# Performance work log

Measured on AMD Instinct MI355X. Metric: run time of the kernel, lower is better.

## Reference

```python
import jax, jax.numpy as jnp
import numpy as np

B, N, C = 8, 4096, 256
HEADS, SR = 8, 4
LN_EPS = 1e-5

def setup_inputs() -> dict:
    key = jax.random.key(0)
    ks = jax.random.split(key, 8)
    std = 0.02
    x = jax.random.normal(ks[0], (B, N, C), dtype=jnp.float32)
    q_w = jax.random.normal(ks[1], (C, C), dtype=jnp.float32) * std          # [in,out]
    kv_w = jax.random.normal(ks[2], (C, 2 * C), dtype=jnp.float32) * std     # [in,2*out]
    fan_out = SR * SR * C
    sr_w = jax.random.normal(ks[3], (C, C, SR, SR), dtype=jnp.float32) * np.sqrt(2.0 / fan_out)  # OIHW
    sr_b = jnp.zeros((C,), dtype=jnp.float32)
    ln_w = jnp.ones((C,), dtype=jnp.float32)
    ln_b = jnp.zeros((C,), dtype=jnp.float32)
    proj_w = jax.random.normal(ks[4], (C, C), dtype=jnp.float32) * std
    proj_b = jnp.zeros((C,), dtype=jnp.float32)
    return {"x": x, "H": 64, "W": 64, "q_w": q_w, "kv_w": kv_w, "sr_w": sr_w,
            "sr_b": sr_b, "ln_w": ln_w, "ln_b": ln_b, "proj_w": proj_w, "proj_b": proj_b}


def reference(x, H, W, q_w, kv_w, sr_w, sr_b, ln_w, ln_b, proj_w, proj_b):
    Bb, Nn, Cc = x.shape
    hd = Cc // HEADS
    scale = hd ** -0.5
    # q: [B, heads, N, hd]
    q = (x @ q_w).reshape(Bb, Nn, HEADS, hd).transpose(0, 2, 1, 3)
    # spatial reduction: conv(stride=sr) + LayerNorm
    x_ = x.transpose(0, 2, 1).reshape(Bb, Cc, H, W)
    x_ = jax.lax.conv_general_dilated(
        x_, sr_w, window_strides=(SR, SR), padding="VALID",
        dimension_numbers=("NCHW", "OIHW", "NCHW")) + sr_b[None, :, None, None]
    x_ = x_.reshape(Bb, Cc, -1).transpose(0, 2, 1)  # [B, Nk, C]
    mu = x_.mean(-1, keepdims=True)
    var = x_.var(-1, keepdims=True)
    x_ = (x_ - mu) * jax.lax.rsqrt(var + LN_EPS) * ln_w + ln_b
    # kv: [B, Nk, 2, heads, hd]
    Nk = x_.shape[1]
    kv = (x_ @ kv_w).reshape(Bb, Nk, 2, HEADS, hd)
    k = kv[:, :, 0].transpose(0, 2, 1, 3)  # [B, heads, Nk, hd]
    v = kv[:, :, 1].transpose(0, 2, 1, 3)  # [B, heads, Nk, hd]
    attn = jnp.einsum("bhnd,bhmd->bhnm", q, k) * scale
    attn = jax.nn.softmax(attn, axis=-1)
    out = jnp.einsum("bhnm,bhmd->bhnd", attn, v)  # [B, heads, N, hd]
    out = out.transpose(0, 2, 1, 3).reshape(Bb, Nn, Cc)
    return out @ proj_w + proj_b
```

## Files before the change

kernel.cpp:

```cpp
#include <hip/hip_runtime.h>
#include <hip/hip_bf16.h>
#include <math.h>

#define DI __device__ __forceinline__

static constexpr float SCALE = 0.17677669529663687f;

typedef short bf16x8 __attribute__((ext_vector_type(8)));
typedef float f32x4 __attribute__((ext_vector_type(4)));

__device__ unsigned short g_qw2[(size_t)256 * 8 * 64];
__device__ unsigned short g_kvw2[(size_t)512 * 8 * 64];
__device__ unsigned short g_pw2[(size_t)256 * 8 * 64];
__device__ unsigned short g_wt2[(size_t)256 * 128 * 64];
__device__ unsigned short g_x2[(size_t)32768 * 8 * 64];
__device__ unsigned short g_ln2[(size_t)2048 * 8 * 64];
__device__ unsigned short g_q[(size_t)64 * 4096 * 32];
__device__ unsigned short g_k[(size_t)64 * 256 * 32];
__device__ unsigned short g_vt[(size_t)64 * 32 * 256];
__device__ unsigned short g_convp[(size_t)16 * 2048 * 256];
__device__ unsigned short g_attnb[(size_t)32768 * 256];

DI float bfbits2f(unsigned short b) { return __uint_as_float(((unsigned)b) << 16); }

DI unsigned short f2bf(float f) {
  unsigned u = __float_as_uint(f);
  unsigned r = (u + 0x7fffu + ((u >> 16) & 1u)) >> 16;
  return (unsigned short)r;
}

DI float4 ld_bf4(const unsigned short* p) {
  ushort4 u = *(const ushort4*)p;
  return make_float4(bfbits2f(u.x), bfbits2f(u.y), bfbits2f(u.z), bfbits2f(u.w));
}

DI float ld1(const void* p, size_t i, int f32) {
  return f32 ? ((const float*)p)[i] : bfbits2f(((const unsigned short*)p)[i]);
}

DI float4 ld4(const void* p, size_t i, int f32) {
  if (f32) return *(const float4*)((const float*)p + i);
  return ld_bf4((const unsigned short*)p + i);
}

typedef const __attribute__((address_space(1))) void* gas_p;
typedef __attribute__((address_space(3))) void* las_p;
DI void gload16(const unsigned short* g, short* l) {
  __builtin_amdgcn_global_load_lds((gas_p)g, (las_p)l, 16, 0, 0);
}

DI int detect_f32(const void* xp) {
  const unsigned* p = (const unsigned*)xp;
  unsigned m0 = 0, m1 = 0;
#pragma unroll
  for (int i = 0; i < 32; ++i) {
    unsigned w = p[i];
    unsigned lo = w & 0x7fffu, hi = (w >> 16) & 0x7fffu;
    m0 = lo > m0 ? lo : m0;
    m1 = hi > m1 ? hi : m1;
  }
  unsigned mm = m0 > m1 ? m0 : m1;
  return mm >= 0x4680u ? 1 : 0;
}

__global__ void k_prep(const void* __restrict__ qw, const void* __restrict__ kvw,
                       const void* __restrict__ pwp, const void* __restrict__ srw,
                       const void* __restrict__ xp) {
  const int f32 = detect_f32(xp);
  int tidg = blockIdx.x * 256 + threadIdx.x;
  float v[8];
  unsigned short* dst;
  if (tidg < 8192) {
    int o = tidg >> 5, w = tidg & 31, k = w * 8;
#pragma unroll
    for (int j = 0; j < 8; ++j) v[j] = ld1(qw, (size_t)(k + j) * 256 + o, f32) * SCALE;
    dst = g_qw2 + ((size_t)o * 8 + (w >> 2)) * 64 + (w & 3) * 8;
  } else if (tidg < 24576) {
    int t = tidg - 8192;
    int o = t >> 5, w = t & 31, k = w * 8;
#pragma unroll
    for (int j = 0; j < 8; ++j) v[j] = ld1(kvw, (size_t)(k + j) * 512 + o, f32);
    dst = g_kvw2 + ((size_t)o * 8 + (w >> 2)) * 64 + (w & 3) * 8;
  } else if (tidg < 32768) {
    int t = tidg - 24576;
    int o = t >> 5, w = t & 31, k = w * 8;
#pragma unroll
    for (int j = 0; j < 8; ++j) v[j] = ld1(pwp, (size_t)(k + j) * 256 + o, f32);
    dst = g_pw2 + ((size_t)o * 8 + (w >> 2)) * 64 + (w & 3) * 8;
  } else if (tidg < 163840) {
    int t = tidg - 32768;
    int o = t >> 9, w = t & 511, k = w * 8;
#pragma unroll
    for (int j = 0; j < 8; ++j) {
      int kk = k + j, tap = kk >> 8, ci = kk & 255;
      v[j] = ld1(srw, (size_t)o * 4096 + (size_t)ci * 16 + tap, f32);
    }
    dst = g_wt2 + ((size_t)o * 128 + (w >> 2)) * 64 + (w & 3) * 8;
  } else {
    int t = tidg - 163840;
    int m = t >> 5, w = t & 31, k = w * 8;
    size_t base = (size_t)m * 256 + k;
    float4 a = ld4(xp, base, f32);
    float4 b = ld4(xp, base + 4, f32);
    v[0] = a.x; v[1] = a.y; v[2] = a.z; v[3] = a.w;
    v[4] = b.x; v[5] = b.y; v[6] = b.z; v[7] = b.w;
    dst = g_x2 + ((size_t)m * 8 + (w >> 2)) * 64 + (w & 3) * 8;
  }
  ushort4 h0, h1, l0, l1;
  h0.x = f2bf(v[0]); l0.x = f2bf(v[0] - bfbits2f(h0.x));
  h0.y = f2bf(v[1]); l0.y = f2bf(v[1] - bfbits2f(h0.y));
  h0.z = f2bf(v[2]); l0.z = f2bf(v[2] - bfbits2f(h0.z));
  h0.w = f2bf(v[3]); l0.w = f2bf(v[3] - bfbits2f(h0.w));
  h1.x = f2bf(v[4]); l1.x = f2bf(v[4] - bfbits2f(h1.x));
  h1.y = f2bf(v[5]); l1.y = f2bf(v[5] - bfbits2f(h1.y));
  h1.z = f2bf(v[6]); l1.z = f2bf(v[6] - bfbits2f(h1.z));
  h1.w = f2bf(v[7]); l1.w = f2bf(v[7] - bfbits2f(h1.w));
  *(ushort4*)dst        = h0;
  *(ushort4*)(dst + 4)  = h1;
  *(ushort4*)(dst + 32) = l0;
  *(ushort4*)(dst + 36) = l1;
}

template <int MODE>
__launch_bounds__(256, 3)
__global__ void k_mgemm(const void* __restrict__ Ax,
                        const void* __restrict__ biasp, void* __restrict__ outp) {
  constexpr bool AH = (MODE != 3);
  constexpr int ASZ = AH ? 4096 : 2048;
  __shared__ __align__(16) short smem[ASZ + 16384];
  short* sa = smem;
  short* sb = smem + ASZ;

  int f32 = 0;
  if constexpr (MODE == 3) f32 = detect_f32(Ax);

  const int tid = threadIdx.x;
  const int m0 = blockIdx.x * 64;
  const int nblk = (MODE == 2) ? blockIdx.y : 0;
  const int z = (MODE == 1) ? blockIdx.z : 0;
  const int wave = tid >> 6, lane = tid & 63;
  const int quad = lane >> 4, l15 = lane & 15;

  const int srow = tid >> 3;
  const int slot = (tid & 7) ^ (srow & 7);

  size_t abase0 = 0, abase1 = 0;
  if constexpr (MODE == 0 || MODE == 2) {
    abase0 = ((size_t)(m0 + srow) * 8) * 64 + slot * 8;
    abase1 = ((size_t)(m0 + 32 + srow) * 8) * 64 + slot * 8;
  } else if constexpr (MODE == 1) {
    const int kh = z >> 2, kw = z & 3;
#pragma unroll
    for (int r = 0; r < 2; ++r) {
      int m = m0 + r * 32 + srow;
      int bb = m >> 8, sp = m & 255;
      int oh = sp >> 4, ow = sp & 15;
      int n = (4 * oh + kh) * 64 + 4 * ow + kw;
      size_t ab = ((size_t)(bb * 4096 + n) * 8) * 64 + slot * 8;
      if (r == 0) abase0 = ab; else abase1 = ab;
    }
  } else {
    int ar = tid >> 2;
    int s3 = (tid & 3) ^ (ar & 3);
    abase0 = (size_t)(m0 + ar) * 256 + s3 * 8;
  }

  const unsigned short* Asrc =
      (MODE == 0 || MODE == 1) ? g_x2 : (MODE == 2) ? g_ln2 : g_attnb;
  const unsigned short* Bsrc = (MODE == 0) ? g_qw2 : (MODE == 1) ? g_wt2
                             : (MODE == 2) ? g_kvw2 : g_pw2;
  constexpr int NKT = (MODE == 1) ? 128 : 8;
  const size_t bbase =
      ((size_t)(nblk * 256 + srow) * NKT + (MODE == 1 ? z * 8 : 0)) * 64 + slot * 8;

  short* adst0 = sa + wave * 512 + lane * 8;
  short* adst1 = sa + 2048 + wave * 512 + lane * 8;
  short* bdst  = sb + wave * 512 + lane * 8;

  int aoff[4], boff[4];
#pragma unroll
  for (int mt = 0; mt < 4; ++mt) {
    int ar = mt * 16 + l15;
    if constexpr (AH) aoff[mt] = ar * 64 + ((quad ^ (ar & 7)) << 3);
    else              aoff[mt] = ar * 32 + ((quad ^ (ar & 3)) << 3);
  }
#pragma unroll
  for (int j = 0; j < 4; ++j) {
    int br = (4 * wave + j) * 16 + l15;
    boff[j] = br * 64 + ((quad ^ (br & 7)) << 3);
  }

  f32x4 acc[4][4] = {};

  for (int it = 0; it < 8; ++it) {
    if constexpr (AH) {
      gload16(Asrc + abase0 + it * 64, adst0);
      gload16(Asrc + abase1 + it * 64, adst1);
    } else {
      gload16(Asrc + abase0 + it * 32, adst0);
    }
#pragma unroll
    for (int r = 0; r < 8; ++r) {
      gload16(Bsrc + bbase + (size_t)r * (32 * NKT * 64) + it * 64, bdst + r * 2048);
    }
    __syncthreads();
#pragma unroll
    for (int mt = 0; mt < 4; ++mt) {
      bf16x8 a_h = *(const bf16x8*)&sa[aoff[mt]];
      bf16x8 a_l;
      if constexpr (AH) a_l = *(const bf16x8*)&sa[aoff[mt] ^ 32];
#pragma unroll
      for (int j = 0; j < 4; ++j) {
        bf16x8 b_h = *(const bf16x8*)&sb[boff[j]];
        bf16x8 b_l = *(const bf16x8*)&sb[boff[j] ^ 32];
        f32x4 c = acc[mt][j];
        c = __builtin_amdgcn_mfma_f32_16x16x32_bf16(a_h, b_h, c, 0, 0, 0);
        if constexpr (AH)
          c = __builtin_amdgcn_mfma_f32_16x16x32_bf16(a_l, b_h, c, 0, 0, 0);
        c = __builtin_amdgcn_mfma_f32_16x16x32_bf16(a_h, b_l, c, 0, 0, 0);
        acc[mt][j] = c;
      }
    }
    __syncthreads();
  }

  const int f32o = f32;
#pragma unroll
  for (int mt = 0; mt < 4; ++mt) {
#pragma unroll
    for (int j = 0; j < 4; ++j) {
#pragma unroll
      for (int r = 0; r < 4; ++r) {
        int m = m0 + mt * 16 + quad * 4 + r;
        int c = nblk * 256 + (4 * wave + j) * 16 + l15;
        float v = acc[mt][j][r];
        if constexpr (MODE == 0) {
          int b = m >> 12, n = m & 4095;
          int h = c >> 5, d = c & 31;
          g_q[(((size_t)(b * 8 + h) * 4096 + n) << 5) + d] = f2bf(v);
        } else if constexpr (MODE == 1) {
          g_convp[((size_t)blockIdx.z * 2048 + m) * 256 + c] = f2bf(v);
        } else if constexpr (MODE == 2) {
          int s = c >> 8, h = (c >> 5) & 7, d = c & 31;
          int bb = m >> 8, nk = m & 255;
          if (s == 0)
            g_k[(((size_t)(bb * 8 + h) * 256 + nk) << 5) + d] = f2bf(v);
          else
            g_vt[(((size_t)(bb * 8 + h) * 32 + d) << 8) + nk] = f2bf(v);
        } else {
          float rr = v + ld1(biasp, c, f32o);
          if (f32o) ((float*)outp)[(size_t)m * 256 + c] = rr;
          else      ((unsigned short*)outp)[(size_t)m * 256 + c] = f2bf(rr);
        }
      }
    }
  }
}

__global__ void k_redln(const void* __restrict__ xp, const void* __restrict__ srb,
                        const void* __restrict__ lw, const void* __restrict__ lb) {
  const int f32 = detect_f32(xp);
  int row = blockIdx.x, t = threadIdx.x;
  size_t idx = (size_t)row * 256 + t;
  float v = 0.f;
#pragma unroll
  for (int z = 0; z < 16; ++z) v += bfbits2f(g_convp[(size_t)z * (2048 * 256) + idx]);
  v += ld1(srb, t, f32);
  float s = v, sq = v * v;
#pragma unroll
  for (int off = 32; off >= 1; off >>= 1) {
    s += __shfl_down(s, off, 64);
    sq += __shfl_down(sq, off, 64);
  }
  __shared__ float rs[4], rq[4];
  int wid = t >> 6;
  if ((t & 63) == 0) { rs[wid] = s; rq[wid] = sq; }
  __syncthreads();
  float st = rs[0] + rs[1] + rs[2] + rs[3];
  float qt = rq[0] + rq[1] + rq[2] + rq[3];
  float mu = st * (1.0f / 256.0f);
  float var = qt * (1.0f / 256.0f) - mu * mu;
  float r = rsqrtf(var + 1e-5f);
  float o = (v - mu) * r * ld1(lw, t, f32) + ld1(lb, t, f32);
  unsigned short hi = f2bf(o);
  size_t dbase = ((size_t)row * 8 + (t >> 5)) * 64 + (t & 31);
  g_ln2[dbase]      = hi;
  g_ln2[dbase + 32] = f2bf(o - bfbits2f(hi));
}

__launch_bounds__(256, 4)
__global__ void k_attn() {
  __shared__ short smem[18688];
  short* sk  = smem;
  short* svt = smem + 10240;

  const int tid = threadIdx.x;
  const int bh = blockIdx.y;
  const int b = bh >> 3, h = bh & 7;

  {
    const uint4* gk = (const uint4*)(g_k + (size_t)bh * 8192);
    const uint4* gv = (const uint4*)(g_vt + (size_t)bh * 8192);
    for (int i = tid; i < 1024; i += 256) {
      int key = i >> 2, part = i & 3;
      *(uint4*)&sk[key * 40 + part * 8] = gk[i];
      int d = i >> 5, off = (i & 31) * 8;
      *(uint4*)&svt[d * 264 + off] = gv[i];
    }
  }
  __syncthreads();

  const int wave = tid >> 6, lane = tid & 63;
  const int quad = lane >> 4, l15 = lane & 15;
  const int n0 = blockIdx.x * 64 + wave * 16;

  bf16x8 qv = *(const bf16x8*)(g_q + ((size_t)bh * 4096 + n0 + l15) * 32 + quad * 8);

  f32x4 sacc[16];
#pragma unroll
  for (int t = 0; t < 16; ++t) {
    bf16x8 kf = *(const bf16x8*)&sk[(t * 16 + l15) * 40 + quad * 8];
    f32x4 c = {0.f, 0.f, 0.f, 0.f};
    sacc[t] = __builtin_amdgcn_mfma_f32_16x16x32_bf16(kf, qv, c, 0, 0, 0);
  }

  float m = sacc[0][0];
#pragma unroll
  for (int t = 0; t < 16; ++t) {
#pragma unroll
    for (int r = 0; r < 4; ++r) m = fmaxf(m, sacc[t][r]);
  }
  m = fmaxf(m, __shfl_xor(m, 16, 64));
  m = fmaxf(m, __shfl_xor(m, 32, 64));

  unsigned plo[16], phi[16];
  float ls = 0.f;
#pragma unroll
  for (int t = 0; t < 16; ++t) {
    unsigned short p0 = f2bf(__expf(sacc[t][0] - m));
    unsigned short p1 = f2bf(__expf(sacc[t][1] - m));
    unsigned short p2 = f2bf(__expf(sacc[t][2] - m));
    unsigned short p3 = f2bf(__expf(sacc[t][3] - m));
    ls += bfbits2f(p0) + bfbits2f(p1) + bfbits2f(p2) + bfbits2f(p3);
    plo[t] = (unsigned)p0 | ((unsigned)p1 << 16);
    phi[t] = (unsigned)p2 | ((unsigned)p3 << 16);
  }
  ls += __shfl_xor(ls, 16, 64);
  ls += __shfl_xor(ls, 32, 64);
  float inv = 1.0f / ls;

  f32x4 o0 = {0.f, 0.f, 0.f, 0.f}, o1 = {0.f, 0.f, 0.f, 0.f};
  const int laneA = ((quad & 1) << 5) + l15;
  const int laneB = laneA + 16;
  const bool hiT = quad >= 2;
#pragma unroll
  for (int c = 0; c < 8; ++c) {
    unsigned a0 = __shfl(plo[2 * c], laneA, 64), b0 = __shfl(plo[2 * c + 1], laneA, 64);
    unsigned a1 = __shfl(phi[2 * c], laneA, 64), b1 = __shfl(phi[2 * c + 1], laneA, 64);
    unsigned a2 = __shfl(plo[2 * c], laneB, 64), b2 = __shfl(plo[2 * c + 1], laneB, 64);
    unsigned a3 = __shfl(phi[2 * c], laneB, 64), b3 = __shfl(phi[2 * c + 1], laneB, 64);
    uint4 pk = make_uint4(hiT ? b0 : a0, hiT ? b1 : a1, hiT ? b2 : a2, hiT ? b3 : a3);
    bf16x8 pf = *(bf16x8*)&pk;
    bf16x8 v0 = *(const bf16x8*)&svt[l15 * 264 + c * 32 + quad * 8];
    bf16x8 v1 = *(const bf16x8*)&svt[(16 + l15) * 264 + c * 32 + quad * 8];
    o0 = __builtin_amdgcn_mfma_f32_16x16x32_bf16(v0, pf, o0, 0, 0, 0);
    o1 = __builtin_amdgcn_mfma_f32_16x16x32_bf16(v1, pf, o1, 0, 0, 0);
  }

  size_t base = ((size_t)(b * 4096 + n0 + l15)) * 256 + h * 32 + quad * 4;
  ushort4 u0, u1;
  u0.x = f2bf(o0[0] * inv); u0.y = f2bf(o0[1] * inv);
  u0.z = f2bf(o0[2] * inv); u0.w = f2bf(o0[3] * inv);
  u1.x = f2bf(o1[0] * inv); u1.y = f2bf(o1[1] * inv);
  u1.z = f2bf(o1[2] * inv); u1.w = f2bf(o1[3] * inv);
  *(ushort4*)&g_attnb[base]      = u0;
  *(ushort4*)&g_attnb[base + 16] = u1;
}

extern "C" void kernel_launch(void* const* d_in, const int* in_sizes, int n_in,
                              void* d_out, int out_size, void* d_ws, size_t ws_size,
                              hipStream_t stream) {
  const void* x   = d_in[0];
  const void* qw  = d_in[3];
  const void* kvw = d_in[4];
  const void* srw = d_in[5];
  const void* srb = d_in[6];
  const void* lnw = d_in[7];
  const void* lnb = d_in[8];
  const void* pw  = d_in[9];
  const void* pb  = d_in[10];

  k_prep<<<4736, 256, 0, stream>>>(qw, kvw, pw, srw, x);
  k_mgemm<0><<<dim3(512, 1), 256, 0, stream>>>(nullptr, nullptr, nullptr);
  k_mgemm<1><<<dim3(32, 1, 16), 256, 0, stream>>>(nullptr, nullptr, nullptr);
  k_redln<<<2048, 256, 0, stream>>>(x, srb, lnw, lnb);
  k_mgemm<2><<<dim3(32, 2), 256, 0, stream>>>(nullptr, nullptr, nullptr);
  k_attn<<<dim3(64, 64), 256, 0, stream>>>();
  k_mgemm<3><<<dim3(512, 1), 256, 0, stream>>>(x, pb, d_out);
}
```

Before: 217.0 us.

## Double-buffer GEMM tiles, merge Q and conv GEMM launches, vectorize LN reduce

The GEMM body becomes a device function that double-buffers its LDS tiles, issuing the next K-slice's loads before the MFMAs on the current one. Separately, the Q projection and conv-partial GEMMs run in one launch of 1024 blocks, which cuts a launch and lets the two fill the device together. The reduce+LayerNorm kernel now handles 8 rows per block with 16-byte vectorized loads and 32-lane shuffles. In exchange, LDS use per block doubles and the launch bound drops to 2 blocks per CU, which lowers occupancy.

```diff
diff --git a/kernel.cpp b/kernel.cpp
--- a/kernel.cpp
+++ b/kernel.cpp
@@ -122,22 +122,14 @@
 }
 
 template <int MODE>
-__launch_bounds__(256, 3)
-__global__ void k_mgemm(const void* __restrict__ Ax,
-                        const void* __restrict__ biasp, void* __restrict__ outp) {
+DI void mgemm_body(short* smem, int bx, int nblk, int z,
+                   const void* __restrict__ biasp, void* __restrict__ outp, int f32) {
   constexpr bool AH = (MODE != 3);
   constexpr int ASZ = AH ? 4096 : 2048;
-  __shared__ __align__(16) short smem[ASZ + 16384];
-  short* sa = smem;
-  short* sb = smem + ASZ;
-
-  int f32 = 0;
-  if constexpr (MODE == 3) f32 = detect_f32(Ax);
+  constexpr int BUF = ASZ + 16384;
 
   const int tid = threadIdx.x;
-  const int m0 = blockIdx.x * 64;
-  const int nblk = (MODE == 2) ? blockIdx.y : 0;
-  const int z = (MODE == 1) ? blockIdx.z : 0;
+  const int m0 = bx * 64;
   const int wave = tid >> 6, lane = tid & 63;
   const int quad = lane >> 4, l15 = lane & 15;
 
@@ -173,10 +165,6 @@
   const size_t bbase =
       ((size_t)(nblk * 256 + srow) * NKT + (MODE == 1 ? z * 8 : 0)) * 64 + slot * 8;
 
-  short* adst0 = sa + wave * 512 + lane * 8;
-  short* adst1 = sa + 2048 + wave * 512 + lane * 8;
-  short* bdst  = sb + wave * 512 + lane * 8;
-
   int aoff[4], boff[4];
 #pragma unroll
   for (int mt = 0; mt < 4; ++mt) {
@@ -190,20 +178,30 @@
     boff[j] = br * 64 + ((quad ^ (br & 7)) << 3);
   }
 
+  auto STAGE = [&](int it, int b) {
+    short* sa = smem + b * BUF;
+    short* sb = sa + ASZ;
+    if constexpr (AH) {
+      gload16(Asrc + abase0 + (size_t)it * 64, sa + tid * 8);
+      gload16(Asrc + abase1 + (size_t)it * 64, sa + 2048 + tid * 8);
+    } else {
+      gload16(Asrc + abase0 + (size_t)it * 32, sa + tid * 8);
+    }
+#pragma unroll
+    for (int r = 0; r < 8; ++r)
+      gload16(Bsrc + bbase + (size_t)r * (32 * NKT * 64) + (size_t)it * 64,
+              sb + tid * 8 + r * 2048);
+  };
+
   f32x4 acc[4][4] = {};
 
+  STAGE(0, 0);
+  __syncthreads();
   for (int it = 0; it < 8; ++it) {
-    if constexpr (AH) {
-      gload16(Asrc + abase0 + it * 64, adst0);
-      gload16(Asrc + abase1 + it * 64, adst1);
-    } else {
-      gload16(Asrc + abase0 + it * 32, adst0);
-    }
-#pragma unroll
-    for (int r = 0; r < 8; ++r) {
-      gload16(Bsrc + bbase + (size_t)r * (32 * NKT * 64) + it * 64, bdst + r * 2048);
-    }
-    __syncthreads();
+    const int cur = it & 1;
+    if (it < 7) STAGE(it + 1, cur ^ 1);
+    const short* sa = smem + cur * BUF;
+    const short* sb = sa + ASZ;
 #pragma unroll
     for (int mt = 0; mt < 4; ++mt) {
       bf16x8 a_h = *(const bf16x8*)&sa[aoff[mt]];
@@ -239,7 +237,7 @@
           int h = c >> 5, d = c & 31;
           g_q[(((size_t)(b * 8 + h) * 4096 + n) << 5) + d] = f2bf(v);
         } else if constexpr (MODE == 1) {
-          g_convp[((size_t)blockIdx.z * 2048 + m) * 256 + c] = f2bf(v);
+          g_convp[((size_t)z * 2048 + m) * 256 + c] = f2bf(v);
         } else if constexpr (MODE == 2) {
           int s = c >> 8, h = (c >> 5) & 7, d = c & 31;
           int bb = m >> 8, nk = m & 255;
@@ -257,35 +255,89 @@
   }
 }
 
+__launch_bounds__(256, 2)
+__global__ void k_mgemm01() {
+  __shared__ __align__(16) short smem[2 * 20480];
+  int bid = blockIdx.x;
+  if (bid < 512) {
+    mgemm_body<0>(smem, bid, 0, 0, nullptr, nullptr, 0);
+  } else {
+    int b2 = bid - 512;
+    mgemm_body<1>(smem, b2 & 31, 0, b2 >> 5, nullptr, nullptr, 0);
+  }
+}
+
+__launch_bounds__(256, 2)
+__global__ void k_mgemm2() {
+  __shared__ __align__(16) short smem[2 * 20480];
+  mgemm_body<2>(smem, blockIdx.x, blockIdx.y, 0, nullptr, nullptr, 0);
+}
+
+__launch_bounds__(256, 2)
+__global__ void k_mgemm3(const void* __restrict__ xp, const void* __restrict__ pb,
+                         void* __restrict__ outp) {
+  __shared__ __align__(16) short smem[2 * 18432];
+  mgemm_body<3>(smem, blockIdx.x, 0, 0, pb, outp, detect_f32(xp));
+}
+
 __global__ void k_redln(const void* __restrict__ xp, const void* __restrict__ srb,
                         const void* __restrict__ lw, const void* __restrict__ lb) {
   const int f32 = detect_f32(xp);
-  int row = blockIdx.x, t = threadIdx.x;
-  size_t idx = (size_t)row * 256 + t;
-  float v = 0.f;
-#pragma unroll
-  for (int z = 0; z < 16; ++z) v += bfbits2f(g_convp[(size_t)z * (2048 * 256) + idx]);
-  v += ld1(srb, t, f32);
-  float s = v, sq = v * v;
-#pragma unroll
-  for (int off = 32; off >= 1; off >>= 1) {
-    s += __shfl_down(s, off, 64);
-    sq += __shfl_down(sq, off, 64);
-  }
-  __shared__ float rs[4], rq[4];
-  int wid = t >> 6;
-  if ((t & 63) == 0) { rs[wid] = s; rq[wid] = sq; }
-  __syncthreads();
-  float st = rs[0] + rs[1] + rs[2] + rs[3];
-  float qt = rq[0] + rq[1] + rq[2] + rq[3];
-  float mu = st * (1.0f / 256.0f);
-  float var = qt * (1.0f / 256.0f) - mu * mu;
-  float r = rsqrtf(var + 1e-5f);
-  float o = (v - mu) * r * ld1(lw, t, f32) + ld1(lb, t, f32);
-  unsigned short hi = f2bf(o);
-  size_t dbase = ((size_t)row * 8 + (t >> 5)) * 64 + (t & 31);
-  g_ln2[dbase]      = hi;
-  g_ln2[dbase + 32] = f2bf(o - bfbits2f(hi));
+  const int t = threadIdx.x;
+  const int row = blockIdx.x * 8 + (t >> 5);
+  const int l32 = t & 31;
+  const int ch0 = l32 * 8;
+  const size_t idx = (size_t)row * 256 + ch0;
+
+  float c[8] = {};
+#pragma unroll
+  for (int zz = 0; zz < 16; ++zz) {
+    uint4 u = *(const uint4*)&g_convp[(size_t)zz * (2048 * 256) + idx];
+    c[0] += __uint_as_float(u.x << 16); c[1] += __uint_as_float(u.x & 0xffff0000u);
+    c[2] += __uint_as_float(u.y << 16); c[3] += __uint_as_float(u.y & 0xffff0000u);
+    c[4] += __uint_as_float(u.z << 16); c[5] += __uint_as_float(u.z & 0xffff0000u);
+    c[6] += __uint_as_float(u.w << 16); c[7] += __uint_as_float(u.w & 0xffff0000u);
+  }
+  float4 b0 = ld4(srb, ch0, f32), b1 = ld4(srb, ch0 + 4, f32);
+  c[0] += b0.x; c[1] += b0.y; c[2] += b0.z; c[3] += b0.w;
+  c[4] += b1.x; c[5] += b1.y; c[6] += b1.z; c[7] += b1.w;
+
+  float s = 0.f, sq = 0.f;
+#pragma unroll
+  for (int j = 0; j < 8; ++j) { s += c[j]; sq += c[j] * c[j]; }
+#pragma unroll
+  for (int off = 16; off >= 1; off >>= 1) {
+    s += __shfl_xor(s, off, 32);
+    sq += __shfl_xor(sq, off, 32);
+  }
+  float mu = s * (1.0f / 256.0f);
+  float var = sq * (1.0f / 256.0f) - mu * mu;
+  float rr = rsqrtf(var + 1e-5f);
+
+  float4 w0 = ld4(lw, ch0, f32), w1 = ld4(lw, ch0 + 4, f32);
+  float4 e0 = ld4(lb, ch0, f32), e1 = ld4(lb, ch0 + 4, f32);
+  float wv[8] = {w0.x, w0.y, w0.z, w0.w, w1.x, w1.y, w1.z, w1.w};
+  float ev[8] = {e0.x, e0.y, e0.z, e0.w, e1.x, e1.y, e1.z, e1.w};
+
+  float o[8];
+#pragma unroll
+  for (int j = 0; j < 8; ++j) o[j] = (c[j] - mu) * rr * wv[j] + ev[j];
+
+  ushort4 h0, h1, l0, l1;
+  h0.x = f2bf(o[0]); l0.x = f2bf(o[0] - bfbits2f(h0.x));
+  h0.y = f2bf(o[1]); l0.y = f2bf(o[1] - bfbits2f(h0.y));
+  h0.z = f2bf(o[2]); l0.z = f2bf(o[2] - bfbits2f(h0.z));
+  h0.w = f2bf(o[3]); l0.w = f2bf(o[3] - bfbits2f(h0.w));
+  h1.x = f2bf(o[4]); l1.x = f2bf(o[4] - bfbits2f(h1.x));
+  h1.y = f2bf(o[5]); l1.y = f2bf(o[5] - bfbits2f(h1.y));
+  h1.z = f2bf(o[6]); l1.z = f2bf(o[6] - bfbits2f(h1.z));
+  h1.w = f2bf(o[7]); l1.w = f2bf(o[7] - bfbits2f(h1.w));
+
+  const size_t dbase = ((size_t)row * 8 + (l32 >> 2)) * 64 + (l32 & 3) * 8;
+  *(ushort4*)&g_ln2[dbase]          = h0;
+  *(ushort4*)&g_ln2[dbase + 4]      = h1;
+  *(ushort4*)&g_ln2[dbase + 32]     = l0;
+  *(ushort4*)&g_ln2[dbase + 36]     = l1;
 }
 
 __launch_bounds__(256, 4)
@@ -391,10 +443,9 @@
   const void* pb  = d_in[10];
 
   k_prep<<<4736, 256, 0, stream>>>(qw, kvw, pw, srw, x);
-  k_mgemm<0><<<dim3(512, 1), 256, 0, stream>>>(nullptr, nullptr, nullptr);
-  k_mgemm<1><<<dim3(32, 1, 16), 256, 0, stream>>>(nullptr, nullptr, nullptr);
-  k_redln<<<2048, 256, 0, stream>>>(x, srb, lnw, lnb);
-  k_mgemm<2><<<dim3(32, 2), 256, 0, stream>>>(nullptr, nullptr, nullptr);
+  k_mgemm01<<<1024, 256, 0, stream>>>();
+  k_redln<<<256, 256, 0, stream>>>(x, srb, lnw, lnb);
+  k_mgemm2<<<dim3(32, 2), 256, 0, stream>>>();
   k_attn<<<dim3(64, 64), 256, 0, stream>>>();
-  k_mgemm<3><<<dim3(512, 1), 256, 0, stream>>>(x, pb, d_out);
-}
+  k_mgemm3<<<512, 256, 0, stream>>>(x, pb, d_out);
+}
```

After: 224.7 us. +3.6%, slower.
